# Performance work log

Hardware: AMD Instinct MI355X
Metric: run time of the kernel (lower is better)

Reference implementation:

```python
import jax, jax.numpy as jnp
import numpy as np

TEMPERATURE = 0.07
EPS = 1e-8  # torch cosine_similarity norm clamp


def setup_inputs() -> dict:
    key = jax.random.key(0)
    k1, k2 = jax.random.split(key)
    B, d = 8192, 256
    X = jax.random.normal(k1, (B, d), dtype=jnp.float32)
    Y = jax.random.normal(k2, (B, d), dtype=jnp.float32)
    return {"X": X, "Y": Y}


def _normalize(v):
    # torch cosine_similarity clamps the norm at eps
    n = jnp.sqrt(jnp.sum(v * v, axis=-1, keepdims=True))
    return v / jnp.maximum(n, EPS)


def reference(X, Y):
    # cosine similarity matrix via normalize + GEMM (same math as broadcasted
    # cosine_similarity(X.unsqueeze(1), Y.unsqueeze(0), dim=-1))
    Xn = _normalize(X)                      # [B, d]
    Yn = _normalize(Y)                      # [B, d]
    logits = (Xn @ Yn.T) / TEMPERATURE      # [B, B]
    # cross_entropy with targets = arange(B): mean of -log_softmax diagonal
    logp = jax.nn.log_softmax(logits, axis=-1)
    loss = -jnp.mean(jnp.diagonal(logp))
    return loss
```

## Files before the change

### kernel.cpp

```cpp
#include <hip/hip_runtime.h>
#include <hip/hip_bf16.h>


typedef __attribute__((ext_vector_type(2)))  float f32x2;
typedef __attribute__((ext_vector_type(4)))  float f32x4;
typedef __attribute__((ext_vector_type(4)))  int   i32x4;
typedef __attribute__((ext_vector_type(8)))  int   i32x8;

#define AS1(p) ((const __attribute__((address_space(1))) void*)(uintptr_t)(p))
#define AS3(p) ((__attribute__((address_space(3))) void*)(uintptr_t)(p))

constexpr int   BROWS = 8192;
constexpr int   DDIM  = 256;
constexpr float kInvT = 14.285714285714286f;
constexpr float kC1   = 20.609929155556622f;
constexpr float kLn2  = 0.6931471805599453f;
constexpr int   kSC   = 0x7F7F7F7F;

#if __has_builtin(__builtin_amdgcn_exp2f)
#define EXP2F(x) __builtin_amdgcn_exp2f(x)
#else
#define EXP2F(x) exp2f(x)
#endif
#if __has_builtin(__builtin_amdgcn_logf)
#define LOG2F(x) __builtin_amdgcn_logf(x)
#else
#define LOG2F(x) log2f(x)
#endif

static __device__ __forceinline__ unsigned f2fp8(float f) {
  unsigned u = __builtin_bit_cast(unsigned, f);
  unsigned s = (u >> 24) & 0x80u;
  float af = __builtin_fabsf(f);
  if (af < 0.015625f) {
    int q = (int)__builtin_rintf(af * 512.0f);
    return s | (unsigned)q;
  }
  unsigned au = u & 0x7FFFFFFFu;
  au += 0x7FFFFu + ((au >> 20) & 1u);
  unsigned e8 = ((au >> 23) - 127u + 7u) & 0xFu;
  unsigned m  = (au >> 20) & 7u;
  return s | (e8 << 3) | m;
}

__global__ __launch_bounds__(256) void nrm_kernel(
    const float* __restrict__ X, const float* __restrict__ Y,
    unsigned int* __restrict__ Xq, unsigned int* __restrict__ Yq,
    float* __restrict__ diag, float* __restrict__ row_sum)
{
  const int wave = threadIdx.x >> 6;
  const int lane = threadIdx.x & 63;
  const int row  = blockIdx.x * 4 + wave;
  const float4 x = *(const float4*)(X + (size_t)row * DDIM + lane * 4);
  const float4 y = *(const float4*)(Y + (size_t)row * DDIM + lane * 4);
  float ssx = x.x*x.x + x.y*x.y + x.z*x.z + x.w*x.w;
  float ssy = y.x*y.x + y.y*y.y + y.z*y.z + y.w*y.w;
  float dot = x.x*y.x + x.y*y.y + x.z*y.z + x.w*y.w;
  #pragma unroll
  for (int m = 1; m < 64; m <<= 1) {
    ssx += __shfl_xor(ssx, m);
    ssy += __shfl_xor(ssy, m);
    dot += __shfl_xor(dot, m);
  }
  const float invx = 1.0f / fmaxf(sqrtf(ssx), 1e-8f);
  const float invy = 1.0f / fmaxf(sqrtf(ssy), 1e-8f);
#if __has_builtin(__builtin_amdgcn_cvt_pk_fp8_f32)
  int xq = __builtin_amdgcn_cvt_pk_fp8_f32(x.x * invx, x.y * invx, 0, false);
  xq     = __builtin_amdgcn_cvt_pk_fp8_f32(x.z * invx, x.w * invx, xq, true);
  int yq = __builtin_amdgcn_cvt_pk_fp8_f32(y.x * invy, y.y * invy, 0, false);
  yq     = __builtin_amdgcn_cvt_pk_fp8_f32(y.z * invy, y.w * invy, yq, true);
#else
  int xq = (int)(f2fp8(x.x*invx) | (f2fp8(x.y*invx) << 8) |
                 (f2fp8(x.z*invx) << 16) | (f2fp8(x.w*invx) << 24));
  int yq = (int)(f2fp8(y.x*invy) | (f2fp8(y.y*invy) << 8) |
                 (f2fp8(y.z*invy) << 16) | (f2fp8(y.w*invy) << 24));
#endif
  Xq[row * 64 + lane] = (unsigned)xq;
  Yq[row * 64 + lane] = (unsigned)yq;
  if (lane == 0) {
    diag[row] = dot * invx * invy * kInvT;
    row_sum[row] = 0.0f;
  }
}

static __device__ __forceinline__ void expflush(f32x4 (&pm)[2], f32x2 (&sm)[2]) {
  #pragma unroll
  for (int n = 0; n < 2; ++n) {
    f32x2 v0 = { pm[n][0], pm[n][1] };
    f32x2 v1 = { pm[n][2], pm[n][3] };
    v0 = v0 * kC1 + (f32x2){-kC1, -kC1};
    v1 = v1 * kC1 + (f32x2){-kC1, -kC1};
    sm[0] += (f32x2){ EXP2F(v0.x), EXP2F(v0.y) };
    sm[1] += (f32x2){ EXP2F(v1.x), EXP2F(v1.y) };
  }
}

static __device__ __forceinline__ void tile_step(
    const char* __restrict__ tb, const int (&bb)[2], const i32x8 (&a)[4][2],
    f32x4 (&cur)[4][2], f32x4 (&prev)[4][2], f32x2 (&sums2)[4][2])
{
  i32x8 b[2];
  __builtin_amdgcn_s_setprio(1);
  #pragma unroll
  for (int n = 0; n < 2; ++n) {
    const i32x4 lo = *(const i32x4*)(tb + (bb[n]));
    const i32x4 hi = *(const i32x4*)(tb + (bb[n] ^ 16));
    b[n] = __builtin_shufflevector(lo, hi, 0, 1, 2, 3, 4, 5, 6, 7);
  }
  #pragma unroll
  for (int m = 0; m < 4; ++m) {
    cur[m][0] = __builtin_amdgcn_mfma_scale_f32_16x16x128_f8f6f4(
        a[m][0], b[0], (f32x4){0.f, 0.f, 0.f, 0.f}, 0, 0, 0, kSC, 0, kSC);
    cur[m][1] = __builtin_amdgcn_mfma_scale_f32_16x16x128_f8f6f4(
        a[m][0], b[1], (f32x4){0.f, 0.f, 0.f, 0.f}, 0, 0, 0, kSC, 0, kSC);
  }
  __builtin_amdgcn_s_setprio(0);
  expflush(prev[0], sums2[0]);
  expflush(prev[1], sums2[1]);
  __builtin_amdgcn_s_setprio(1);
  #pragma unroll
  for (int n = 0; n < 2; ++n) {
    const i32x4 lo = *(const i32x4*)(tb + (bb[n] ^ 128));
    const i32x4 hi = *(const i32x4*)(tb + (bb[n] ^ 144));
    b[n] = __builtin_shufflevector(lo, hi, 0, 1, 2, 3, 4, 5, 6, 7);
  }
  #pragma unroll
  for (int m = 0; m < 4; ++m) {
    cur[m][0] = __builtin_amdgcn_mfma_scale_f32_16x16x128_f8f6f4(
        a[m][1], b[0], cur[m][0], 0, 0, 0, kSC, 0, kSC);
    cur[m][1] = __builtin_amdgcn_mfma_scale_f32_16x16x128_f8f6f4(
        a[m][1], b[1], cur[m][1], 0, 0, 0, kSC, 0, kSC);
  }
  __builtin_amdgcn_s_setprio(0);
  expflush(prev[2], sums2[2]);
  expflush(prev[3], sums2[3]);
}

__global__ __launch_bounds__(256, 2) void logits_kernel(
    const unsigned char* __restrict__ Xq,
    const unsigned char* __restrict__ Yq,
    float* __restrict__ row_sum)
{
  __shared__ char lds[4 * 8192];
  const int tid  = threadIdx.x;
  const int lane = tid & 63;
  const int wave = tid >> 6;
  const int l15  = lane & 15;
  const int g    = lane >> 4;

  const int bid  = blockIdx.x;
  const int xcd  = bid & 7;
  const int idx  = bid >> 3;
  const int panel = idx & 31;
  const int split = xcd * 4 + (idx >> 5);

  const int rowbase = panel * 256 + wave * 64;
  const char* Xb = (const char*)Xq;
  const char* Yb = (const char*)Yq + (size_t)split * (256 * 256);

  i32x8 a[4][2];
  #pragma unroll
  for (int m = 0; m < 4; ++m) {
    const char* rp = Xb + (size_t)(rowbase + m * 16 + l15) * 256 + g * 32;
    a[m][0] = *(const i32x8*)(rp);
    a[m][1] = *(const i32x8*)(rp + 128);
  }

  f32x2 sums2[4][2];
  #pragma unroll
  for (int m = 0; m < 4; ++m) {
    sums2[m][0] = (f32x2){0.f, 0.f};
    sums2[m][1] = (f32x2){0.f, 0.f};
  }

  int bb[2];
  #pragma unroll
  for (int n = 0; n < 2; ++n)
    bb[n] = (n * 16 + l15) * 256 + (((2 * g) ^ l15) << 4);

  auto stage = [&](int t, int buf) {
    const char* Yt = Yb + (size_t)t * 8192;
    char* db = lds + buf * 8192;
    #pragma unroll
    for (int s = 0; s < 2; ++s) {
      const int portion = (s * 4 + wave) * 1024;
      const int L = portion + lane * 16;
      const int src = (L & ~255) | ((L & 255) ^ (((L >> 8) & 15) << 4));
      __builtin_amdgcn_global_load_lds(AS1(Yt + src), AS3(db + portion), 16, 0, 0);
    }
  };

  f32x4 accA[4][2], accB[4][2];
  #pragma unroll
  for (int m = 0; m < 4; ++m)
    #pragma unroll
    for (int n = 0; n < 2; ++n) {
      accA[m][n] = (f32x4){0.f, 0.f, 0.f, 0.f};
      const float ni = -__builtin_inff();
      accB[m][n] = (f32x4){ni, ni, ni, ni};
    }

  stage(0, 0);
  stage(1, 1);
  stage(2, 2);
  #pragma unroll 1
  for (int p = 0; p < 4; ++p) {
    const int t = 2 * p;
    if (p < 3) asm volatile("s_waitcnt vmcnt(4)" ::: "memory");
    else       asm volatile("s_waitcnt vmcnt(2)" ::: "memory");
    __builtin_amdgcn_s_barrier();
    if (t + 3 < 8) stage(t + 3, (t + 3) & 3);
    tile_step(lds + (t & 3) * 8192, bb, a, accA, accB, sums2);
    if (p < 3) asm volatile("s_waitcnt vmcnt(4)" ::: "memory");
    else       asm volatile("s_waitcnt vmcnt(0)" ::: "memory");
    __builtin_amdgcn_s_barrier();
    if (t + 4 < 8) stage(t + 4, (t + 4) & 3);
    tile_step(lds + ((t + 1) & 3) * 8192, bb, a, accB, accA, sums2);
  }
  #pragma unroll
  for (int m = 0; m < 4; ++m)
    expflush(accB[m], sums2[m]);

  #pragma unroll
  for (int m = 0; m < 4; ++m)
    #pragma unroll
    for (int h = 0; h < 2; ++h)
      #pragma unroll
      for (int r2 = 0; r2 < 2; ++r2) {
        float s = (r2 == 0) ? sums2[m][h].x : sums2[m][h].y;
        s += __shfl_xor(s, 1);
        s += __shfl_xor(s, 2);
        s += __shfl_xor(s, 4);
        s += __shfl_xor(s, 8);
        if (l15 == 0)
          atomicAdd(row_sum + rowbase + m * 16 + g * 4 + h * 2 + r2, s);
      }
}

__global__ __launch_bounds__(1024) void loss_kernel(
    const float* __restrict__ row_sum, const float* __restrict__ diag,
    float* __restrict__ out)
{
  const int t = threadIdx.x;
  double acc = 0.0;
  #pragma unroll
  for (int h = 0; h < 2; ++h) {
    const int i = h * 4096 + t * 4;
    const float4 s = *(const float4*)(row_sum + i);
    const float4 d = *(const float4*)(diag + i);
    acc += (double)(kInvT + LOG2F(s.x) * kLn2 - d.x);
    acc += (double)(kInvT + LOG2F(s.y) * kLn2 - d.y);
    acc += (double)(kInvT + LOG2F(s.z) * kLn2 - d.z);
    acc += (double)(kInvT + LOG2F(s.w) * kLn2 - d.w);
  }
  #pragma unroll
  for (int m = 1; m < 64; m <<= 1) acc += __shfl_xor(acc, m);
  __shared__ double red[16];
  if ((t & 63) == 0) red[t >> 6] = acc;
  __syncthreads();
  if (t == 0) {
    double tot = 0.0;
    #pragma unroll
    for (int w = 0; w < 16; ++w) tot += red[w];
    out[0] = (float)(tot / (double)BROWS);
  }
}

extern "C" void kernel_launch(void* const* d_in, const int* in_sizes, int n_in,
                              void* d_out, int out_size, void* d_ws, size_t ws_size,
                              hipStream_t stream) {
  (void)in_sizes; (void)n_in; (void)out_size; (void)ws_size;
  const float* X = (const float*)d_in[0];
  const float* Y = (const float*)d_in[1];
  char* w = (char*)d_ws;
  unsigned int* Xq = (unsigned int*)(w);
  unsigned int* Yq = (unsigned int*)(w + (2u << 20));
  float* diag    = (float*)(w + (4u << 20));
  float* row_sum = (float*)(w + (4u << 20) + (32u << 10));

  nrm_kernel<<<BROWS / 4, 256, 0, stream>>>(X, Y, Xq, Yq, diag, row_sum);
  logits_kernel<<<1024, 256, 0, stream>>>((const unsigned char*)Xq,
                                          (const unsigned char*)Yq, row_sum);
  loss_kernel<<<1, 1024, 0, stream>>>(row_sum, diag, (float*)d_out);
}
```

Measured before the change: 40.80 us.

## Pre-swizzle fp8 operands into MFMA fragment order and drop LDS staging

The normalization kernel now writes the quantized X and Y in a layout that matches the MFMA operand fragments, so each wave loads its A and B fragments straight from global memory with coalesced 16-byte loads. The logits kernel drops the LDS ring buffer, the barriers and the software-pipelined exp/MFMA interleave. Each wave now owns an independent 64x128 tile. The grid doubles and the occupancy target rises to three blocks per CU. This removes LDS traffic and block-level synchronization, but B fragments are no longer shared across waves through LDS, which adds global/L2 traffic, and exp work is no longer overlapped explicitly with MFMA.

```diff
diff --git a/kernel.cpp b/kernel.cpp
--- a/kernel.cpp
+++ b/kernel.cpp
@@ -6,9 +6,6 @@
 typedef __attribute__((ext_vector_type(4)))  float f32x4;
 typedef __attribute__((ext_vector_type(4)))  int   i32x4;
 typedef __attribute__((ext_vector_type(8)))  int   i32x8;
-
-#define AS1(p) ((const __attribute__((address_space(1))) void*)(uintptr_t)(p))
-#define AS3(p) ((__attribute__((address_space(3))) void*)(uintptr_t)(p))
 
 constexpr int   BROWS = 8192;
 constexpr int   DDIM  = 256;
@@ -75,96 +72,52 @@
   int yq = (int)(f2fp8(y.x*invy) | (f2fp8(y.y*invy) << 8) |
                  (f2fp8(y.z*invy) << 16) | (f2fp8(y.w*invy) << 24));
 #endif
-  Xq[row * 64 + lane] = (unsigned)xq;
-  Yq[row * 64 + lane] = (unsigned)yq;
+  const int idx = (row >> 4) * 1024 + (lane >> 5) * 512 + ((lane >> 2) & 1) * 256
+                + ((lane >> 3) & 3) * 64 + (row & 15) * 4 + (lane & 3);
+  Xq[idx] = (unsigned)xq;
+  Yq[idx] = (unsigned)yq;
   if (lane == 0) {
     diag[row] = dot * invx * invy * kInvT;
     row_sum[row] = 0.0f;
   }
 }
 
-static __device__ __forceinline__ void expflush(f32x4 (&pm)[2], f32x2 (&sm)[2]) {
-  #pragma unroll
-  for (int n = 0; n < 2; ++n) {
-    f32x2 v0 = { pm[n][0], pm[n][1] };
-    f32x2 v1 = { pm[n][2], pm[n][3] };
-    v0 = v0 * kC1 + (f32x2){-kC1, -kC1};
-    v1 = v1 * kC1 + (f32x2){-kC1, -kC1};
-    sm[0] += (f32x2){ EXP2F(v0.x), EXP2F(v0.y) };
-    sm[1] += (f32x2){ EXP2F(v1.x), EXP2F(v1.y) };
-  }
-}
-
-static __device__ __forceinline__ void tile_step(
-    const char* __restrict__ tb, const int (&bb)[2], const i32x8 (&a)[4][2],
-    f32x4 (&cur)[4][2], f32x4 (&prev)[4][2], f32x2 (&sums2)[4][2])
-{
-  i32x8 b[2];
-  __builtin_amdgcn_s_setprio(1);
-  #pragma unroll
-  for (int n = 0; n < 2; ++n) {
-    const i32x4 lo = *(const i32x4*)(tb + (bb[n]));
-    const i32x4 hi = *(const i32x4*)(tb + (bb[n] ^ 16));
-    b[n] = __builtin_shufflevector(lo, hi, 0, 1, 2, 3, 4, 5, 6, 7);
-  }
-  #pragma unroll
-  for (int m = 0; m < 4; ++m) {
-    cur[m][0] = __builtin_amdgcn_mfma_scale_f32_16x16x128_f8f6f4(
-        a[m][0], b[0], (f32x4){0.f, 0.f, 0.f, 0.f}, 0, 0, 0, kSC, 0, kSC);
-    cur[m][1] = __builtin_amdgcn_mfma_scale_f32_16x16x128_f8f6f4(
-        a[m][0], b[1], (f32x4){0.f, 0.f, 0.f, 0.f}, 0, 0, 0, kSC, 0, kSC);
-  }
-  __builtin_amdgcn_s_setprio(0);
-  expflush(prev[0], sums2[0]);
-  expflush(prev[1], sums2[1]);
-  __builtin_amdgcn_s_setprio(1);
-  #pragma unroll
-  for (int n = 0; n < 2; ++n) {
-    const i32x4 lo = *(const i32x4*)(tb + (bb[n] ^ 128));
-    const i32x4 hi = *(const i32x4*)(tb + (bb[n] ^ 144));
-    b[n] = __builtin_shufflevector(lo, hi, 0, 1, 2, 3, 4, 5, 6, 7);
-  }
-  #pragma unroll
-  for (int m = 0; m < 4; ++m) {
-    cur[m][0] = __builtin_amdgcn_mfma_scale_f32_16x16x128_f8f6f4(
-        a[m][1], b[0], cur[m][0], 0, 0, 0, kSC, 0, kSC);
-    cur[m][1] = __builtin_amdgcn_mfma_scale_f32_16x16x128_f8f6f4(
-        a[m][1], b[1], cur[m][1], 0, 0, 0, kSC, 0, kSC);
-  }
-  __builtin_amdgcn_s_setprio(0);
-  expflush(prev[2], sums2[2]);
-  expflush(prev[3], sums2[3]);
-}
-
-__global__ __launch_bounds__(256, 2) void logits_kernel(
+static __device__ __forceinline__ void expq(const f32x4& pv, f32x2 (&sm)[2]) {
+  f32x2 v0 = { pv[0], pv[1] };
+  f32x2 v1 = { pv[2], pv[3] };
+  v0 = v0 * kC1 + (f32x2){-kC1, -kC1};
+  v1 = v1 * kC1 + (f32x2){-kC1, -kC1};
+  sm[0] += (f32x2){ EXP2F(v0.x), EXP2F(v0.y) };
+  sm[1] += (f32x2){ EXP2F(v1.x), EXP2F(v1.y) };
+}
+
+__global__ __launch_bounds__(256, 3) void logits_kernel(
     const unsigned char* __restrict__ Xq,
     const unsigned char* __restrict__ Yq,
     float* __restrict__ row_sum)
 {
-  __shared__ char lds[4 * 8192];
-  const int tid  = threadIdx.x;
-  const int lane = tid & 63;
-  const int wave = tid >> 6;
+  const int lane = threadIdx.x & 63;
+  const int wv   = threadIdx.x >> 6;
+  const int bid  = blockIdx.x;
+  const int xcd  = bid & 7;
+  const int widx = (bid >> 3) * 4 + wv;
+  const int mg   = widx & 127;
+  const int ng   = xcd * 8 + (widx >> 7);
   const int l15  = lane & 15;
   const int g    = lane >> 4;
 
-  const int bid  = blockIdx.x;
-  const int xcd  = bid & 7;
-  const int idx  = bid >> 3;
-  const int panel = idx & 31;
-  const int split = xcd * 4 + (idx >> 5);
-
-  const int rowbase = panel * 256 + wave * 64;
-  const char* Xb = (const char*)Xq;
-  const char* Yb = (const char*)Yq + (size_t)split * (256 * 256);
+  const char* Xb = (const char*)Xq + (size_t)mg * 16384 + lane * 16;
+  const char* Yb = (const char*)Yq + (size_t)ng * 32768 + lane * 16;
 
   i32x8 a[4][2];
   #pragma unroll
-  for (int m = 0; m < 4; ++m) {
-    const char* rp = Xb + (size_t)(rowbase + m * 16 + l15) * 256 + g * 32;
-    a[m][0] = *(const i32x8*)(rp);
-    a[m][1] = *(const i32x8*)(rp + 128);
-  }
+  for (int m = 0; m < 4; ++m)
+    #pragma unroll
+    for (int kb = 0; kb < 2; ++kb) {
+      const i32x4 lo = *(const i32x4*)(Xb + m * 4096 + kb * 2048);
+      const i32x4 hi = *(const i32x4*)(Xb + m * 4096 + kb * 2048 + 1024);
+      a[m][kb] = __builtin_shufflevector(lo, hi, 0, 1, 2, 3, 4, 5, 6, 7);
+    }
 
   f32x2 sums2[4][2];
   #pragma unroll
@@ -173,53 +126,29 @@
     sums2[m][1] = (f32x2){0.f, 0.f};
   }
 
-  int bb[2];
-  #pragma unroll
-  for (int n = 0; n < 2; ++n)
-    bb[n] = (n * 16 + l15) * 256 + (((2 * g) ^ l15) << 4);
-
-  auto stage = [&](int t, int buf) {
-    const char* Yt = Yb + (size_t)t * 8192;
-    char* db = lds + buf * 8192;
-    #pragma unroll
-    for (int s = 0; s < 2; ++s) {
-      const int portion = (s * 4 + wave) * 1024;
-      const int L = portion + lane * 16;
-      const int src = (L & ~255) | ((L & 255) ^ (((L >> 8) & 15) << 4));
-      __builtin_amdgcn_global_load_lds(AS1(Yt + src), AS3(db + portion), 16, 0, 0);
+  #pragma unroll
+  for (int nf = 0; nf < 8; ++nf) {
+    f32x4 acc[4];
+    __builtin_amdgcn_s_setprio(1);
+    #pragma unroll
+    for (int kb = 0; kb < 2; ++kb) {
+      const i32x4 lo = *(const i32x4*)(Yb + nf * 4096 + kb * 2048);
+      const i32x4 hi = *(const i32x4*)(Yb + nf * 4096 + kb * 2048 + 1024);
+      const i32x8 b = __builtin_shufflevector(lo, hi, 0, 1, 2, 3, 4, 5, 6, 7);
+      #pragma unroll
+      for (int m = 0; m < 4; ++m) {
+        acc[m] = (kb == 0)
+          ? __builtin_amdgcn_mfma_scale_f32_16x16x128_f8f6f4(
+                a[m][0], b, (f32x4){0.f, 0.f, 0.f, 0.f}, 0, 0, 0, kSC, 0, kSC)
+          : __builtin_amdgcn_mfma_scale_f32_16x16x128_f8f6f4(
+                a[m][1], b, acc[m], 0, 0, 0, kSC, 0, kSC);
+      }
     }
-  };
-
-  f32x4 accA[4][2], accB[4][2];
-  #pragma unroll
-  for (int m = 0; m < 4; ++m)
-    #pragma unroll
-    for (int n = 0; n < 2; ++n) {
-      accA[m][n] = (f32x4){0.f, 0.f, 0.f, 0.f};
-      const float ni = -__builtin_inff();
-      accB[m][n] = (f32x4){ni, ni, ni, ni};
-    }
-
-  stage(0, 0);
-  stage(1, 1);
-  stage(2, 2);
-  #pragma unroll 1
-  for (int p = 0; p < 4; ++p) {
-    const int t = 2 * p;
-    if (p < 3) asm volatile("s_waitcnt vmcnt(4)" ::: "memory");
-    else       asm volatile("s_waitcnt vmcnt(2)" ::: "memory");
-    __builtin_amdgcn_s_barrier();
-    if (t + 3 < 8) stage(t + 3, (t + 3) & 3);
-    tile_step(lds + (t & 3) * 8192, bb, a, accA, accB, sums2);
-    if (p < 3) asm volatile("s_waitcnt vmcnt(4)" ::: "memory");
-    else       asm volatile("s_waitcnt vmcnt(0)" ::: "memory");
-    __builtin_amdgcn_s_barrier();
-    if (t + 4 < 8) stage(t + 4, (t + 4) & 3);
-    tile_step(lds + ((t + 1) & 3) * 8192, bb, a, accB, accA, sums2);
-  }
-  #pragma unroll
-  for (int m = 0; m < 4; ++m)
-    expflush(accB[m], sums2[m]);
+    __builtin_amdgcn_s_setprio(0);
+    #pragma unroll
+    for (int m = 0; m < 4; ++m)
+      expq(acc[m], sums2[m]);
+  }
 
   #pragma unroll
   for (int m = 0; m < 4; ++m)
@@ -233,7 +162,7 @@
         s += __shfl_xor(s, 4);
         s += __shfl_xor(s, 8);
         if (l15 == 0)
-          atomicAdd(row_sum + rowbase + m * 16 + g * 4 + h * 2 + r2, s);
+          atomicAdd(row_sum + mg * 64 + m * 16 + g * 4 + h * 2 + r2, s);
       }
 }
 
@@ -279,7 +208,7 @@
   float* row_sum = (float*)(w + (4u << 20) + (32u << 10));
 
   nrm_kernel<<<BROWS / 4, 256, 0, stream>>>(X, Y, Xq, Yq, diag, row_sum);
-  logits_kernel<<<1024, 256, 0, stream>>>((const unsigned char*)Xq,
+  logits_kernel<<<2048, 256, 0, stream>>>((const unsigned char*)Xq,
                                           (const unsigned char*)Yq, row_sum);
   loss_kernel<<<1, 1024, 0, stream>>>(row_sum, diag, (float*)d_out);
 }
```

New measurement: 120.5 us. +195.4%, slower.
